# Performance work log

Measured on AMD Instinct MI355X. Metric: run time of the kernel, lower is better.

## Reference

```python
import jax, jax.numpy as jnp
import numpy as np

NUM_EXPERTS = 64
TOP_K = 8
NORM_TOPK_PROB = True


def setup_inputs() -> dict:
    key = jax.random.key(0)
    k1, k2 = jax.random.split(key)
    hidden_states = jax.random.normal(k1, (8192, 4096), dtype=jnp.float32)
    gate_w = jax.random.normal(k2, (NUM_EXPERTS, 4096), dtype=jnp.float32) * (1.0 / np.sqrt(4096))
    return {"hidden_states": hidden_states, "gate_w": gate_w}


def reference(hidden_states, gate_w):
    # router_logits: (T, E) = hidden @ gate_w.T
    router_logits = jnp.einsum('th,eh->te', hidden_states, gate_w)
    # softmax in float32 (matches F.softmax(..., dtype=torch.float32))
    router_probs = jax.nn.softmax(router_logits.astype(jnp.float32), axis=-1)
    # top-k selection (descending, like torch.topk)
    expert_weights, expert_indices = jax.lax.top_k(router_probs, TOP_K)
    if NORM_TOPK_PROB:
        expert_weights = expert_weights / jnp.sum(expert_weights, axis=-1, keepdims=True)
    expert_weights = expert_weights.astype(hidden_states.dtype)
    # load-balancing loss: N_e * sum_i f_i * p_i
    num_tokens = router_probs.shape[0]
    one_hot = jax.nn.one_hot(expert_indices, NUM_EXPERTS, dtype=jnp.float32)  # (T, K, E)
    tokens_per_expert = one_hot.sum(axis=(0, 1))                              # (E,)
    f = tokens_per_expert / (num_tokens * TOP_K)
    p = router_probs.mean(axis=0)
    aux_loss = NUM_EXPERTS * jnp.sum(f * p)
    return (expert_weights, expert_indices, aux_loss)
```

## Files before the change

### kernel.cpp

```cpp
#include <hip/hip_runtime.h>
#include <math.h>

#define HDIM 4096
#define NEXP 64
#define NTOK 8192
#define KSPLIT 8
#define KSLICE (HDIM / KSPLIT)
#define NCHUNK (KSLICE / 32)
#define NKC (HDIM / 32)
#define AUXF 1024
#define TPW 2
#define BT_TERM (NKC * 4 * 64 * 8)
#define BT_KC (4 * 64 * 8)

typedef short short8 __attribute__((ext_vector_type(8)));
typedef float f32x4 __attribute__((ext_vector_type(4)));

union i4s8 { int4 i; short8 s; };

__device__ __forceinline__ void split2x3(float x0, float x1, int& h, int& md, int& lo) {
  unsigned u0 = __float_as_uint(x0), u1 = __float_as_uint(x1);
  unsigned h0 = u0 & 0xFFFF0000u, h1 = u1 & 0xFFFF0000u;
  float r0 = x0 - __uint_as_float(h0);
  float r1 = x1 - __uint_as_float(h1);
  unsigned m0 = __float_as_uint(r0) & 0xFFFF0000u;
  unsigned m1 = __float_as_uint(r1) & 0xFFFF0000u;
  float s0 = r0 - __uint_as_float(m0);
  float s1 = r1 - __uint_as_float(m1);
  h  = (int)((h0 >> 16) | h1);
  md = (int)((m0 >> 16) | m1);
  lo = (int)((__float_as_uint(s0) >> 16) | (__float_as_uint(s1) & 0xFFFF0000u));
}

__device__ __forceinline__ void split8(const float4& p0, const float4& p1,
                                       short8& h8, short8& m8, short8& l8) {
  i4s8 h, m, l;
  split2x3(p0.x, p0.y, h.i.x, m.i.x, l.i.x);
  split2x3(p0.z, p0.w, h.i.y, m.i.y, l.i.y);
  split2x3(p1.x, p1.y, h.i.z, m.i.z, l.i.z);
  split2x3(p1.z, p1.w, h.i.w, m.i.w, l.i.w);
  h8 = h.s; m8 = m.s; l8 = l.s;
}

__global__ __launch_bounds__(256) void prep_k(const float* __restrict__ W,
                                              short* __restrict__ Bs,
                                              float* __restrict__ auxbuf) {
  if (blockIdx.x == 128) {
#pragma unroll
    for (int j = 0; j < 4; ++j) auxbuf[j * 256 + threadIdx.x] = 0.f;
    return;
  }
  const int g = blockIdx.x * 256 + threadIdx.x;
  const int n = g >> 9;
  const int k8 = g & 511;
  const float4 p0 = *(const float4*)&W[(size_t)n * HDIM + k8 * 8];
  const float4 p1 = *(const float4*)&W[(size_t)n * HDIM + k8 * 8 + 4];
  short8 h8, m8, l8;
  split8(p0, p1, h8, m8, l8);
  const int kc = k8 >> 2, quad = k8 & 3;
  const size_t o = (((size_t)kc * 4 + quad) * 64 + n) * 8;
  *(short8*)&Bs[o] = h8;
  *(short8*)&Bs[o + BT_TERM] = m8;
  *(short8*)&Bs[o + 2 * BT_TERM] = l8;
}

__global__ __launch_bounds__(256) void gemm_k(const float* __restrict__ A,
                                              const short* __restrict__ Bs,
                                              float* __restrict__ Lp,
                                              int atomic_mode) {
  const int tid = threadIdx.x;
  const int wave = tid >> 6, lane = tid & 63;
  const int l15 = lane & 15, quad = lane >> 4;
  const int m_base = blockIdx.x * 128 + wave * 32;
  const int kb = blockIdx.y;
  float* Lout = Lp + (atomic_mode ? (size_t)0 : (size_t)kb * NTOK * NEXP);

  const float* a0 = A + (size_t)(m_base + l15) * HDIM + kb * KSLICE + quad * 8;
  const float* a1 = a0 + (size_t)16 * HDIM;
  const short* bbase = Bs + ((size_t)(kb * NCHUNK) * 4 + quad) * 512 + l15 * 8;

  f32x4 acc[2][4];
#pragma unroll
  for (int mt = 0; mt < 2; ++mt)
#pragma unroll
    for (int nt = 0; nt < 4; ++nt) acc[mt][nt] = (f32x4){0.f, 0.f, 0.f, 0.f};

  float4 ra[2][2][2];
  auto loadA = [&](int buf, int i) {
    ra[buf][0][0] = *(const float4*)(a0 + i * 32);
    ra[buf][0][1] = *(const float4*)(a0 + i * 32 + 4);
    ra[buf][1][0] = *(const float4*)(a1 + i * 32);
    ra[buf][1][1] = *(const float4*)(a1 + i * 32 + 4);
  };
  loadA(0, 0);

#pragma unroll 2
  for (int i = 0; i < NCHUNK; ++i) {
    const int cur = i & 1;
    if (i + 1 < NCHUNK) loadA(cur ^ 1, i + 1);
    short8 fa[2][3];
#pragma unroll
    for (int mt = 0; mt < 2; ++mt)
      split8(ra[cur][mt][0], ra[cur][mt][1], fa[mt][0], fa[mt][1], fa[mt][2]);
    const short* bc = bbase + (size_t)i * BT_KC;
#pragma unroll
    for (int nt = 0; nt < 4; ++nt) {
      const short8 bh = *(const short8*)(bc + nt * 128);
      const short8 bm = *(const short8*)(bc + nt * 128 + BT_TERM);
      const short8 bl = *(const short8*)(bc + nt * 128 + 2 * BT_TERM);
#pragma unroll
      for (int mt = 0; mt < 2; ++mt) {
        f32x4 c = acc[mt][nt];
        c = __builtin_amdgcn_mfma_f32_16x16x32_bf16(fa[mt][0], bh, c, 0, 0, 0);
        c = __builtin_amdgcn_mfma_f32_16x16x32_bf16(fa[mt][0], bm, c, 0, 0, 0);
        c = __builtin_amdgcn_mfma_f32_16x16x32_bf16(fa[mt][1], bh, c, 0, 0, 0);
        c = __builtin_amdgcn_mfma_f32_16x16x32_bf16(fa[mt][0], bl, c, 0, 0, 0);
        c = __builtin_amdgcn_mfma_f32_16x16x32_bf16(fa[mt][2], bh, c, 0, 0, 0);
        c = __builtin_amdgcn_mfma_f32_16x16x32_bf16(fa[mt][1], bm, c, 0, 0, 0);
        acc[mt][nt] = c;
      }
    }
  }

#pragma unroll
  for (int mt = 0; mt < 2; ++mt)
#pragma unroll
    for (int nt = 0; nt < 4; ++nt)
#pragma unroll
      for (int r = 0; r < 4; ++r) {
        const int m = m_base + mt * 16 + quad * 4 + r;
        const int n = nt * 16 + l15;
        if (atomic_mode) atomicAdd(&Lout[(size_t)m * NEXP + n], acc[mt][nt][r]);
        else Lout[(size_t)m * NEXP + n] = acc[mt][nt][r];
      }
}

__global__ __launch_bounds__(256) void topk_k(const float* __restrict__ Lp, int nsl,
                                              float* __restrict__ out,
                                              float* __restrict__ auxbuf) {
  __shared__ float sl[4][64];
  __shared__ float s_aux[128];
  const int tid = threadIdx.x;
  const int wave = tid >> 6, lane = tid & 63;
  if (tid < 128) s_aux[tid] = 0.f;
  __syncthreads();

  for (int it = 0; it < TPW; ++it) {
    const int t = (blockIdx.x * 4 + wave) * TPW + it;
    float x = 0.f;
    for (int s = 0; s < nsl; ++s)
      x += Lp[(size_t)s * (NTOK * NEXP) + (size_t)t * NEXP + lane];
    sl[wave][lane] = x;

    float mx = x;
#pragma unroll
    for (int off = 32; off >= 1; off >>= 1)
      mx = fmaxf(mx, __shfl_xor(mx, off, 64));
    const float e = __expf(x - mx);
    float ssum = e;
#pragma unroll
    for (int off = 32; off >= 1; off >>= 1) ssum += __shfl_xor(ssum, off, 64);
    const float prob = e / ssum;

    __syncthreads();

    int cnt = 0;
#pragma unroll
    for (int c = 0; c < 4; ++c) {
      const float4 v0 = *(const float4*)&sl[wave][c * 16 + 0];
      const float4 v1 = *(const float4*)&sl[wave][c * 16 + 4];
      const float4 v2 = *(const float4*)&sl[wave][c * 16 + 8];
      const float4 v3 = *(const float4*)&sl[wave][c * 16 + 12];
      const float xv[16] = {v0.x, v0.y, v0.z, v0.w, v1.x, v1.y, v1.z, v1.w,
                            v2.x, v2.y, v2.z, v2.w, v3.x, v3.y, v3.z, v3.w};
#pragma unroll
      for (int j = 0; j < 16; ++j) {
        const int jj = c * 16 + j;
        cnt += (xv[j] > x) || (xv[j] == x && jj < lane);
      }
    }

    float tp = (cnt < 8) ? prob : 0.f;
    float tsum = tp;
#pragma unroll
    for (int off = 32; off >= 1; off >>= 1) tsum += __shfl_xor(tsum, off, 64);

    const int dst = cnt << 2;
    const float pv = __uint_as_float(
        (unsigned)__builtin_amdgcn_ds_permute(dst, (int)__float_as_uint(prob)));
    const int pi = __builtin_amdgcn_ds_permute(dst, lane);
    if (lane < 8) {
      out[(size_t)t * 8 + lane] = pv / tsum;
      out[(size_t)NTOK * 8 + (size_t)t * 8 + lane] = (float)pi;
    }
    atomicAdd(&s_aux[lane], prob);
    if (cnt < 8) atomicAdd(&s_aux[64 + lane], 1.f);
  }
  __syncthreads();
  if (tid < 128) atomicAdd(&auxbuf[(blockIdx.x & 7) * 128 + tid], s_aux[tid]);
}

__global__ void aux_k(const float* __restrict__ auxbuf, float* __restrict__ out) {
  const int e = threadIdx.x;
  float p = 0.f, f = 0.f;
#pragma unroll
  for (int c = 0; c < 8; ++c) {
    p += auxbuf[c * 128 + e];
    f += auxbuf[c * 128 + 64 + e];
  }
  p *= (1.f / (float)NTOK);
  f *= (1.f / ((float)NTOK * 8.f));
  float v = f * p;
#pragma unroll
  for (int off = 32; off >= 1; off >>= 1) v += __shfl_xor(v, off, 64);
  if (e == 0) out[2 * NTOK * 8] = 64.f * v;
}

extern "C" void kernel_launch(void* const* d_in, const int* in_sizes, int n_in,
                              void* d_out, int out_size, void* d_ws, size_t ws_size,
                              hipStream_t stream) {
  const float* hidden = (const float*)d_in[0];
  const float* gate = (const float*)d_in[1];
  float* out = (float*)d_out;
  float* ws = (float*)d_ws;
  float* auxbuf = ws;

  const size_t full_need =
      (size_t)AUXF * 4 + (size_t)KSPLIT * NTOK * NEXP * 4 + (size_t)3 * BT_TERM * 2;
  const int atomic_mode = (ws_size < full_need) ? 1 : 0;
  const int nsl = atomic_mode ? 1 : KSPLIT;
  float* slices = ws + AUXF;
  short* Bs = (short*)(ws + AUXF + (size_t)nsl * NTOK * NEXP);

  if (atomic_mode)
    hipMemsetAsync(slices, 0, (size_t)NTOK * NEXP * 4, stream);

  prep_k<<<129, 256, 0, stream>>>(gate, Bs, auxbuf);
  gemm_k<<<dim3(64, KSPLIT), 256, 0, stream>>>(hidden, Bs, slices, atomic_mode);
  topk_k<<<NTOK / (4 * TPW), 256, 0, stream>>>(slices, nsl, out, auxbuf);
  aux_k<<<1, 64, 0, stream>>>(auxbuf, out);
}
```

Baseline: 227.8 us.

## Halve per-wave M tile, double grid, and deepen A prefetch with pre-split fragments

```diff
diff --git a/kernel.cpp b/kernel.cpp
--- a/kernel.cpp
+++ b/kernel.cpp
@@ -64,75 +64,73 @@
   *(short8*)&Bs[o + 2 * BT_TERM] = l8;
 }
 
-__global__ __launch_bounds__(256) void gemm_k(const float* __restrict__ A,
-                                              const short* __restrict__ Bs,
-                                              float* __restrict__ Lp,
-                                              int atomic_mode) {
+__global__ __launch_bounds__(256, 4) void gemm_k(const float* __restrict__ A,
+                                                 const short* __restrict__ Bs,
+                                                 float* __restrict__ Lp,
+                                                 int atomic_mode) {
   const int tid = threadIdx.x;
   const int wave = tid >> 6, lane = tid & 63;
   const int l15 = lane & 15, quad = lane >> 4;
-  const int m_base = blockIdx.x * 128 + wave * 32;
+  const int m_base = blockIdx.x * 64 + wave * 16;
   const int kb = blockIdx.y;
   float* Lout = Lp + (atomic_mode ? (size_t)0 : (size_t)kb * NTOK * NEXP);
 
   const float* a0 = A + (size_t)(m_base + l15) * HDIM + kb * KSLICE + quad * 8;
-  const float* a1 = a0 + (size_t)16 * HDIM;
   const short* bbase = Bs + ((size_t)(kb * NCHUNK) * 4 + quad) * 512 + l15 * 8;
 
-  f32x4 acc[2][4];
-#pragma unroll
-  for (int mt = 0; mt < 2; ++mt)
-#pragma unroll
-    for (int nt = 0; nt < 4; ++nt) acc[mt][nt] = (f32x4){0.f, 0.f, 0.f, 0.f};
-
-  float4 ra[2][2][2];
+  f32x4 acc[4];
+#pragma unroll
+  for (int nt = 0; nt < 4; ++nt) acc[nt] = (f32x4){0.f, 0.f, 0.f, 0.f};
+
+  float4 ra[2][2];
   auto loadA = [&](int buf, int i) {
-    ra[buf][0][0] = *(const float4*)(a0 + i * 32);
-    ra[buf][0][1] = *(const float4*)(a0 + i * 32 + 4);
-    ra[buf][1][0] = *(const float4*)(a1 + i * 32);
-    ra[buf][1][1] = *(const float4*)(a1 + i * 32 + 4);
+    ra[buf][0] = *(const float4*)(a0 + i * 32);
+    ra[buf][1] = *(const float4*)(a0 + i * 32 + 4);
   };
+
+  short8 fa_cur[3], fa_next[3];
   loadA(0, 0);
+  loadA(1, 1);
+  split8(ra[0][0], ra[0][1], fa_cur[0], fa_cur[1], fa_cur[2]);
 
 #pragma unroll 2
   for (int i = 0; i < NCHUNK; ++i) {
-    const int cur = i & 1;
-    if (i + 1 < NCHUNK) loadA(cur ^ 1, i + 1);
-    short8 fa[2][3];
-#pragma unroll
-    for (int mt = 0; mt < 2; ++mt)
-      split8(ra[cur][mt][0], ra[cur][mt][1], fa[mt][0], fa[mt][1], fa[mt][2]);
     const short* bc = bbase + (size_t)i * BT_KC;
+    short8 bh[4], bm[4], bl[4];
 #pragma unroll
     for (int nt = 0; nt < 4; ++nt) {
-      const short8 bh = *(const short8*)(bc + nt * 128);
-      const short8 bm = *(const short8*)(bc + nt * 128 + BT_TERM);
-      const short8 bl = *(const short8*)(bc + nt * 128 + 2 * BT_TERM);
-#pragma unroll
-      for (int mt = 0; mt < 2; ++mt) {
-        f32x4 c = acc[mt][nt];
-        c = __builtin_amdgcn_mfma_f32_16x16x32_bf16(fa[mt][0], bh, c, 0, 0, 0);
-        c = __builtin_amdgcn_mfma_f32_16x16x32_bf16(fa[mt][0], bm, c, 0, 0, 0);
-        c = __builtin_amdgcn_mfma_f32_16x16x32_bf16(fa[mt][1], bh, c, 0, 0, 0);
-        c = __builtin_amdgcn_mfma_f32_16x16x32_bf16(fa[mt][0], bl, c, 0, 0, 0);
-        c = __builtin_amdgcn_mfma_f32_16x16x32_bf16(fa[mt][2], bh, c, 0, 0, 0);
-        c = __builtin_amdgcn_mfma_f32_16x16x32_bf16(fa[mt][1], bm, c, 0, 0, 0);
-        acc[mt][nt] = c;
-      }
-    }
-  }
-
-#pragma unroll
-  for (int mt = 0; mt < 2; ++mt)
-#pragma unroll
-    for (int nt = 0; nt < 4; ++nt)
-#pragma unroll
-      for (int r = 0; r < 4; ++r) {
-        const int m = m_base + mt * 16 + quad * 4 + r;
-        const int n = nt * 16 + l15;
-        if (atomic_mode) atomicAdd(&Lout[(size_t)m * NEXP + n], acc[mt][nt][r]);
-        else Lout[(size_t)m * NEXP + n] = acc[mt][nt][r];
-      }
+      bh[nt] = *(const short8*)(bc + nt * 128);
+      bm[nt] = *(const short8*)(bc + nt * 128 + BT_TERM);
+      bl[nt] = *(const short8*)(bc + nt * 128 + 2 * BT_TERM);
+    }
+    if (i + 2 < NCHUNK) loadA(i & 1, i + 2);
+    if (i + 1 < NCHUNK)
+      split8(ra[(i + 1) & 1][0], ra[(i + 1) & 1][1],
+             fa_next[0], fa_next[1], fa_next[2]);
+#pragma unroll
+    for (int nt = 0; nt < 4; ++nt) {
+      f32x4 c = acc[nt];
+      c = __builtin_amdgcn_mfma_f32_16x16x32_bf16(fa_cur[0], bh[nt], c, 0, 0, 0);
+      c = __builtin_amdgcn_mfma_f32_16x16x32_bf16(fa_cur[0], bm[nt], c, 0, 0, 0);
+      c = __builtin_amdgcn_mfma_f32_16x16x32_bf16(fa_cur[1], bh[nt], c, 0, 0, 0);
+      c = __builtin_amdgcn_mfma_f32_16x16x32_bf16(fa_cur[0], bl[nt], c, 0, 0, 0);
+      c = __builtin_amdgcn_mfma_f32_16x16x32_bf16(fa_cur[2], bh[nt], c, 0, 0, 0);
+      c = __builtin_amdgcn_mfma_f32_16x16x32_bf16(fa_cur[1], bm[nt], c, 0, 0, 0);
+      acc[nt] = c;
+    }
+#pragma unroll
+    for (int r = 0; r < 3; ++r) fa_cur[r] = fa_next[r];
+  }
+
+#pragma unroll
+  for (int nt = 0; nt < 4; ++nt)
+#pragma unroll
+    for (int r = 0; r < 4; ++r) {
+      const int m = m_base + quad * 4 + r;
+      const int n = nt * 16 + l15;
+      if (atomic_mode) atomicAdd(&Lout[(size_t)m * NEXP + n], acc[nt][r]);
+      else Lout[(size_t)m * NEXP + n] = acc[nt][r];
+    }
 }
 
 __global__ __launch_bounds__(256) void topk_k(const float* __restrict__ Lp, int nsl,
@@ -236,7 +234,7 @@
     hipMemsetAsync(slices, 0, (size_t)NTOK * NEXP * 4, stream);
 
   prep_k<<<129, 256, 0, stream>>>(gate, Bs, auxbuf);
-  gemm_k<<<dim3(64, KSPLIT), 256, 0, stream>>>(hidden, Bs, slices, atomic_mode);
+  gemm_k<<<dim3(128, KSPLIT), 256, 0, stream>>>(hidden, Bs, slices, atomic_mode);
   topk_k<<<NTOK / (4 * TPW), 256, 0, stream>>>(slices, nsl, out, auxbuf);
   aux_k<<<1, 64, 0, stream>>>(auxbuf, out);
 }
```

Measured after the change: 238.1 us. 1.05x slower.
